# Optimization experiments

Hardware: AMD Instinct MI355X
Metric: run time of the kernel (lower is better)

Reference implementation:

```python
import jax, jax.numpy as jnp
from jax import lax
import numpy as np

B, C, H, W = 16, 128, 128, 128


def setup_inputs() -> dict:
    key = jax.random.key(0)
    k1, k2, k3 = jax.random.split(key, 3)
    x = jax.random.normal(k1, (B, C, H, W), dtype=jnp.float32)
    # depthwise Conv2d(C, C, k=3, padding=1, groups=C): weight (C, 1, 3, 3), bias (C,)
    dw_weight = jax.random.normal(k2, (C, 1, 3, 3), dtype=jnp.float32) * 0.05
    dw_bias = jax.random.normal(k3, (C,), dtype=jnp.float32) * 0.05
    gamma = jnp.zeros((1,), dtype=jnp.float32)  # nn.Parameter(torch.zeros(1))
    return {"x": x, "dw_weight": dw_weight, "dw_bias": dw_bias, "gamma": gamma}


def reference(x, dw_weight, dw_bias, gamma):
    b, c, h, w = x.shape
    f = x.reshape(b, c, h * w)                      # [B, C, N]
    # channel-attention Gram matrix: [B, C, C]
    atten = jnp.einsum('bcn,bdn->bcd', f, f)
    # max-subtract (not softmax): rowwise max minus scores
    atten = jnp.max(atten, axis=-1, keepdims=True) - atten
    # project back to spatial: [B, C, N] -> [B, C, H, W]
    atten = jnp.einsum('bcd,bdn->bcn', atten, f).reshape(b, c, h, w)
    # depthwise 3x3 conv, padding=1
    atten = lax.conv_general_dilated(
        atten, dw_weight,
        window_strides=(1, 1), padding='SAME',
        dimension_numbers=('NCHW', 'OIHW', 'NCHW'),
        feature_group_count=c,
    ) + dw_bias[None, :, None, None]
    # softmax over last dim (W), as torch Softmax(dim=-1) on 4D tensor
    atten = jax.nn.softmax(atten, axis=-1)
    out = gamma * atten + x
    return (out, atten)
```

## Files before the change

kernel.cpp:

```cpp
#include <hip/hip_runtime.h>

#define Bn 16
#define Cn 128
#define Hn 128
#define Wn 128
#define Nn (Hn * Wn)
#define KSPLIT 32

typedef __attribute__((ext_vector_type(8))) short bf16x8;
typedef __attribute__((ext_vector_type(4))) float f32x4;

__device__ __forceinline__ unsigned short bfh(float f) {
    unsigned u = __float_as_uint(f);
    u += 0x7FFFu + ((u >> 16) & 1u);
    return (unsigned short)(u >> 16);
}
__device__ __forceinline__ float bf2f(unsigned short h) {
    return __uint_as_float(((unsigned)h) << 16);
}

__device__ __forceinline__ bf16x8 ldfrag(const unsigned short* S, int row, int quad) {
    return *(const bf16x8*)(S + row * 40 + quad * 8);
}

__global__ __launch_bounds__(256) void colsum_kernel(const float* __restrict__ x,
                                                     float* __restrict__ colsum) {
    const int b = blockIdx.x >> 4;
    const int nt = blockIdx.x & 15;
    const int n4 = (nt << 10) + (threadIdx.x << 2);
    const float* __restrict__ fb = x + (size_t)b * Cn * Nn;
    float4 s = {0.f, 0.f, 0.f, 0.f};
    for (int c = 0; c < Cn; ++c) {
        const float4 v = *(const float4*)(fb + (size_t)c * Nn + n4);
        s.x += v.x; s.y += v.y; s.z += v.z; s.w += v.w;
    }
    *(float4*)(colsum + (size_t)b * Nn + n4) = s;
}

__global__ __launch_bounds__(256, 2) void gram_mfma(const float* __restrict__ x,
                                                    float* __restrict__ Gp) {
    const int bid = blockIdx.x;
    const int ks = bid & 31;
    const int b = bid >> 5;
    const float* __restrict__ fb = x + (size_t)b * Cn * Nn;
    const int k0 = ks << 9;

    __shared__ __align__(16) unsigned short Shi[128 * 40];
    __shared__ __align__(16) unsigned short Slo[128 * 40];

    const int tid = threadIdx.x;
    const int wave = tid >> 6, lane = tid & 63;
    const int m = lane & 15, quad = lane >> 4;
    const int wr = (wave >> 1) << 6;
    const int wc = (wave & 1) << 6;

    f32x4 acc[4][4];
#pragma unroll
    for (int i = 0; i < 4; ++i)
#pragma unroll
        for (int j = 0; j < 4; ++j) acc[i][j] = (f32x4){0.f, 0.f, 0.f, 0.f};

    for (int ck = 0; ck < 512; ck += 32) {
        __syncthreads();
#pragma unroll
        for (int p = 0; p < 4; ++p) {
            const int q = tid + (p << 8);
            const int c = q >> 3;
            const int k4 = (q & 7) << 2;
            const float4 v = *(const float4*)(fb + (size_t)c * Nn + k0 + ck + k4);
            const float f0[4] = {v.x, v.y, v.z, v.w};
            unsigned short h[4], l[4];
#pragma unroll
            for (int e = 0; e < 4; ++e) {
                h[e] = bfh(f0[e]);
                l[e] = bfh(f0[e] - bf2f(h[e]));
            }
            *(ushort4*)(Shi + c * 40 + k4) = make_ushort4(h[0], h[1], h[2], h[3]);
            *(ushort4*)(Slo + c * 40 + k4) = make_ushort4(l[0], l[1], l[2], l[3]);
        }
        __syncthreads();

        bf16x8 Ah[4], Al[4], Bh[4], Bl[4];
#pragma unroll
        for (int i = 0; i < 4; ++i) {
            Ah[i] = ldfrag(Shi, wr + (i << 4) + m, quad);
            Al[i] = ldfrag(Slo, wr + (i << 4) + m, quad);
            Bh[i] = ldfrag(Shi, wc + (i << 4) + m, quad);
            Bl[i] = ldfrag(Slo, wc + (i << 4) + m, quad);
        }
#pragma unroll
        for (int i = 0; i < 4; ++i)
#pragma unroll
            for (int j = 0; j < 4; ++j) {
                acc[i][j] = __builtin_amdgcn_mfma_f32_16x16x32_bf16(Ah[i], Bh[j], acc[i][j], 0, 0, 0);
                acc[i][j] = __builtin_amdgcn_mfma_f32_16x16x32_bf16(Ah[i], Bl[j], acc[i][j], 0, 0, 0);
                acc[i][j] = __builtin_amdgcn_mfma_f32_16x16x32_bf16(Al[i], Bh[j], acc[i][j], 0, 0, 0);
            }
    }

    float* __restrict__ Gb = Gp + (((size_t)ks * Bn + b) << 14);
#pragma unroll
    for (int i = 0; i < 4; ++i)
#pragma unroll
        for (int j = 0; j < 4; ++j)
#pragma unroll
            for (int r = 0; r < 4; ++r) {
                const int row = wr + (i << 4) + (quad << 2) + r;
                const int col = wc + (j << 4) + m;
                Gb[(row << 7) + col] = acc[i][j][r];
            }
}

__global__ __launch_bounds__(128) void prep_kernel(const float* __restrict__ Gp,
                                                   unsigned short* __restrict__ Lhi,
                                                   unsigned short* __restrict__ Llo,
                                                   float* __restrict__ rowmax,
                                                   float* __restrict__ gdiag) {
    const int row = blockIdx.x;
    const int b = row >> 7;
    const int c = row & 127;
    const int t = threadIdx.x;

    const float* __restrict__ p = Gp + (((size_t)b) << 14) + (c << 7) + t;
    float v = 0.0f;
#pragma unroll
    for (int ks = 0; ks < KSPLIT; ++ks)
        v += p[(size_t)ks * ((size_t)Bn << 14)];

    __shared__ float red[128];
    red[t] = v;
    __syncthreads();
#pragma unroll
    for (int s = 64; s > 0; s >>= 1) {
        if (t < s) red[t] = fmaxf(red[t], red[t + s]);
        __syncthreads();
    }
    if (t == 0) rowmax[row] = red[0];
    if (t == c) gdiag[row] = v;
    const float l = (t == c) ? 0.0f : -v;
    const unsigned short h = bfh(l);
    Lhi[(size_t)row * Cn + t] = h;
    Llo[(size_t)row * Cn + t] = bfh(l - bf2f(h));
}

__global__ __launch_bounds__(256, 2) void ymm_mfma(const unsigned short* __restrict__ Lhi,
                                                   const unsigned short* __restrict__ Llo,
                                                   const float* __restrict__ x,
                                                   const float* __restrict__ colsum,
                                                   const float* __restrict__ rowmax,
                                                   const float* __restrict__ gdiag,
                                                   float* __restrict__ Y) {
    const int bid = blockIdx.x;
    const int xcd = bid & 7;
    const int j2 = bid >> 3;
    const int b = (xcd << 1) + (j2 & 1);
    const int nt = j2 >> 1;
    const int n0 = nt << 7;

    const float* __restrict__ fb = x + (size_t)b * Cn * Nn;
    const unsigned short* __restrict__ Lhb = Lhi + (size_t)b * Cn * Cn;
    const unsigned short* __restrict__ Llb = Llo + (size_t)b * Cn * Cn;

    __shared__ __align__(16) unsigned short SAh[128 * 40];
    __shared__ __align__(16) unsigned short SAl[128 * 40];
    __shared__ __align__(16) unsigned short SBh[128 * 40];
    __shared__ __align__(16) unsigned short SBl[128 * 40];

    const int tid = threadIdx.x;
    const int wave = tid >> 6, lane = tid & 63;
    const int m = lane & 15, quad = lane >> 4;
    const int wrc = (wave >> 1) << 6;
    const int wn = (wave & 1) << 6;

    f32x4 acc[4][4];
#pragma unroll
    for (int i = 0; i < 4; ++i)
#pragma unroll
        for (int j = 0; j < 4; ++j) acc[i][j] = (f32x4){0.f, 0.f, 0.f, 0.f};

    for (int dd = 0; dd < Cn; dd += 32) {
        __syncthreads();
#pragma unroll
        for (int p = 0; p < 4; ++p) {
            const int q = tid + (p << 8);
            const int c = q >> 3;
            const int d4 = (q & 7) << 2;
            *(ushort4*)(SAh + c * 40 + d4) = *(const ushort4*)(Lhb + (size_t)c * Cn + dd + d4);
            *(ushort4*)(SAl + c * 40 + d4) = *(const ushort4*)(Llb + (size_t)c * Cn + dd + d4);
        }
#pragma unroll
        for (int p = 0; p < 4; ++p) {
            const int q = tid + (p << 8);
            const int nl = q & 127;
            const int d4 = (q >> 7) << 2;
            unsigned short h[4], l[4];
#pragma unroll
            for (int e = 0; e < 4; ++e) {
                const float f0 = fb[(size_t)(dd + d4 + e) * Nn + n0 + nl];
                h[e] = bfh(f0);
                l[e] = bfh(f0 - bf2f(h[e]));
            }
            *(ushort4*)(SBh + nl * 40 + d4) = make_ushort4(h[0], h[1], h[2], h[3]);
            *(ushort4*)(SBl + nl * 40 + d4) = make_ushort4(l[0], l[1], l[2], l[3]);
        }
        __syncthreads();

        bf16x8 Ah[4], Al[4], Bh[4], Bl[4];
#pragma unroll
        for (int i = 0; i < 4; ++i) {
            Ah[i] = ldfrag(SAh, wrc + (i << 4) + m, quad);
            Al[i] = ldfrag(SAl, wrc + (i << 4) + m, quad);
            Bh[i] = ldfrag(SBh, wn + (i << 4) + m, quad);
            Bl[i] = ldfrag(SBl, wn + (i << 4) + m, quad);
        }
#pragma unroll
        for (int i = 0; i < 4; ++i)
#pragma unroll
            for (int j = 0; j < 4; ++j) {
                acc[i][j] = __builtin_amdgcn_mfma_f32_16x16x32_bf16(Ah[i], Bh[j], acc[i][j], 0, 0, 0);
                acc[i][j] = __builtin_amdgcn_mfma_f32_16x16x32_bf16(Ah[i], Bl[j], acc[i][j], 0, 0, 0);
                acc[i][j] = __builtin_amdgcn_mfma_f32_16x16x32_bf16(Al[i], Bh[j], acc[i][j], 0, 0, 0);
            }
    }

    float* __restrict__ Yb = Y + (size_t)b * Cn * Nn;
#pragma unroll
    for (int i = 0; i < 4; ++i)
#pragma unroll
        for (int r = 0; r < 4; ++r) {
            const int c = wrc + (i << 4) + (quad << 2) + r;
            const float rm = rowmax[(b << 7) + c];
            const float gd = gdiag[(b << 7) + c];
#pragma unroll
            for (int j = 0; j < 4; ++j) {
                const int n = n0 + wn + (j << 4) + m;
                const float cs = colsum[(size_t)b * Nn + n];
                const float fv = fb[(size_t)c * Nn + n];
                Yb[(size_t)c * Nn + n] = fmaf(rm, cs, fmaf(-gd, fv, acc[i][j][r]));
            }
        }
}

__global__ __launch_bounds__(256) void conv_softmax_kernel(const float* __restrict__ Yin,
                                                           const float* __restrict__ wgt,
                                                           const float* __restrict__ bias,
                                                           const float* __restrict__ x,
                                                           const float* __restrict__ gamma,
                                                           float* __restrict__ out,
                                                           float* __restrict__ atten) {
    const int pid = blockIdx.x;
    const int c = pid & (Cn - 1);
    const size_t pbase = (size_t)pid * Nn;

    __shared__ __align__(16) float P[128][131];

    const int tid = threadIdx.x;

#pragma unroll
    for (int p = 0; p < 16; ++p) {
        const int q = tid + (p << 8);
        const int row = q >> 5;
        const int c4 = (q & 31) << 2;
        const float4 v = *(const float4*)(Yin + pbase + (size_t)row * Wn + c4);
        P[row][1 + c4 + 0] = v.x; P[row][1 + c4 + 1] = v.y;
        P[row][1 + c4 + 2] = v.z; P[row][1 + c4 + 3] = v.w;
    }
    if (tid < 128) { P[tid][0] = 0.0f; P[tid][129] = 0.0f; }

    float wk[9];
#pragma unroll
    for (int i = 0; i < 9; ++i) wk[i] = wgt[c * 9 + i];
    const float bs = bias[c];
    const float g = gamma[0];

    __syncthreads();

    const int h = tid >> 1;
    const int c0 = (tid & 1) << 6;

    float acc0[32], acc1[32];
#pragma unroll
    for (int w = 0; w < 32; ++w) { acc0[w] = bs; acc1[w] = bs; }

#pragma unroll
    for (int chunk = 0; chunk < 2; ++chunk) {
        float* acc = chunk ? acc1 : acc0;
        const int cb = c0 + (chunk << 5);
#pragma unroll
        for (int kh = 0; kh < 3; ++kh) {
            const int hh = h + kh - 1;
            if (hh < 0 || hh >= Hn) continue;
            float r[34];
#pragma unroll
            for (int i = 0; i < 34; ++i) r[i] = P[hh][cb + i];
            const float w0 = wk[kh * 3 + 0], w1 = wk[kh * 3 + 1], w2 = wk[kh * 3 + 2];
#pragma unroll
            for (int w = 0; w < 32; ++w)
                acc[w] = fmaf(w0, r[w], fmaf(w1, r[w + 1], fmaf(w2, r[w + 2], acc[w])));
        }
    }

    float m = -1e30f;
#pragma unroll
    for (int w = 0; w < 32; ++w) m = fmaxf(m, fmaxf(acc0[w], acc1[w]));
    m = fmaxf(m, __shfl_xor(m, 1));
    float s = 0.0f;
#pragma unroll
    for (int w = 0; w < 32; ++w) { acc0[w] = __expf(acc0[w] - m); s += acc0[w]; }
#pragma unroll
    for (int w = 0; w < 32; ++w) { acc1[w] = __expf(acc1[w] - m); s += acc1[w]; }
    s += __shfl_xor(s, 1);
    const float inv = 1.0f / s;

    __syncthreads();

#pragma unroll
    for (int w = 0; w < 32; ++w) {
        P[h][1 + c0 + w] = acc0[w] * inv;
        P[h][1 + c0 + 32 + w] = acc1[w] * inv;
    }
    __syncthreads();

#pragma unroll
    for (int p = 0; p < 16; ++p) {
        const int q = tid + (p << 8);
        const int row = q >> 5;
        const int c4 = (q & 31) << 2;
        float4 a;
        a.x = P[row][1 + c4 + 0]; a.y = P[row][1 + c4 + 1];
        a.z = P[row][1 + c4 + 2]; a.w = P[row][1 + c4 + 3];
        const float4 xv = *(const float4*)(x + pbase + (size_t)row * Wn + c4);
        float4 o;
        o.x = fmaf(g, a.x, xv.x); o.y = fmaf(g, a.y, xv.y);
        o.z = fmaf(g, a.z, xv.z); o.w = fmaf(g, a.w, xv.w);
        *(float4*)(atten + pbase + (size_t)row * Wn + c4) = a;
        *(float4*)(out + pbase + (size_t)row * Wn + c4) = o;
    }
}

extern "C" void kernel_launch(void* const* d_in, const int* in_sizes, int n_in,
                              void* d_out, int out_size, void* d_ws, size_t ws_size,
                              hipStream_t stream) {
    const float* x     = (const float*)d_in[0];
    const float* wgt   = (const float*)d_in[1];
    const float* bias  = (const float*)d_in[2];
    const float* gamma = (const float*)d_in[3];

    float* out   = (float*)d_out;
    float* atten = out + (size_t)Bn * Cn * Nn;

    float* Gp = (float*)d_ws;
    float* colsum = Gp + ((size_t)KSPLIT * Bn << 14);
    unsigned short* Lhi = (unsigned short*)(colsum + (size_t)Bn * Nn);
    unsigned short* Llo = Lhi + (size_t)Bn * Cn * Cn;
    float* rowmax = atten;
    float* gdiag  = atten + 2048;

    float* Y = out;

    colsum_kernel<<<Bn * 16, 256, 0, stream>>>(x, colsum);
    gram_mfma<<<Bn * 32, 256, 0, stream>>>(x, Gp);
    prep_kernel<<<Bn * Cn, 128, 0, stream>>>(Gp, Lhi, Llo, rowmax, gdiag);
    ymm_mfma<<<Bn * 128, 256, 0, stream>>>(Lhi, Llo, x, colsum, rowmax, gdiag, Y);
    conv_softmax_kernel<<<Bn * Cn, 256, 0, stream>>>(Y, wgt, bias, x, gamma, out, atten);
}
```

Measured before the change: 525.5 us.

## Fuse column-sum into Gram kernel and load A fragments directly from global

Drops the separate colsum kernel and computes per-column channel sums inside gram_mfma from the float4 values it already loads, reducing them with cross-lane shuffles and a small shared buffer. This removes one full read pass over x (about 128 MB). In ymm_mfma, the L matrix fragments are now read straight from global memory into registers instead of being staged through shared memory. That cuts LDS traffic and shared-memory footprint, at the cost of more uncoalesced global loads from the small L matrices, which are likely cached.

```diff
diff --git a/kernel.cpp b/kernel.cpp
--- a/kernel.cpp
+++ b/kernel.cpp
@@ -23,22 +23,9 @@
     return *(const bf16x8*)(S + row * 40 + quad * 8);
 }
 
-__global__ __launch_bounds__(256) void colsum_kernel(const float* __restrict__ x,
-                                                     float* __restrict__ colsum) {
-    const int b = blockIdx.x >> 4;
-    const int nt = blockIdx.x & 15;
-    const int n4 = (nt << 10) + (threadIdx.x << 2);
-    const float* __restrict__ fb = x + (size_t)b * Cn * Nn;
-    float4 s = {0.f, 0.f, 0.f, 0.f};
-    for (int c = 0; c < Cn; ++c) {
-        const float4 v = *(const float4*)(fb + (size_t)c * Nn + n4);
-        s.x += v.x; s.y += v.y; s.z += v.z; s.w += v.w;
-    }
-    *(float4*)(colsum + (size_t)b * Nn + n4) = s;
-}
-
 __global__ __launch_bounds__(256, 2) void gram_mfma(const float* __restrict__ x,
-                                                    float* __restrict__ Gp) {
+                                                    float* __restrict__ Gp,
+                                                    float* __restrict__ colsum) {
     const int bid = blockIdx.x;
     const int ks = bid & 31;
     const int b = bid >> 5;
@@ -47,6 +34,7 @@
 
     __shared__ __align__(16) unsigned short Shi[128 * 40];
     __shared__ __align__(16) unsigned short Slo[128 * 40];
+    __shared__ float csumW[4][512];
 
     const int tid = threadIdx.x;
     const int wave = tid >> 6, lane = tid & 63;
@@ -62,12 +50,14 @@
 
     for (int ck = 0; ck < 512; ck += 32) {
         __syncthreads();
+        float4 cs = {0.f, 0.f, 0.f, 0.f};
 #pragma unroll
         for (int p = 0; p < 4; ++p) {
             const int q = tid + (p << 8);
             const int c = q >> 3;
             const int k4 = (q & 7) << 2;
             const float4 v = *(const float4*)(fb + (size_t)c * Nn + k0 + ck + k4);
+            cs.x += v.x; cs.y += v.y; cs.z += v.z; cs.w += v.w;
             const float f0[4] = {v.x, v.y, v.z, v.w};
             unsigned short h[4], l[4];
 #pragma unroll
@@ -77,6 +67,17 @@
             }
             *(ushort4*)(Shi + c * 40 + k4) = make_ushort4(h[0], h[1], h[2], h[3]);
             *(ushort4*)(Slo + c * 40 + k4) = make_ushort4(l[0], l[1], l[2], l[3]);
+        }
+#pragma unroll
+        for (int s = 8; s < 64; s <<= 1) {
+            cs.x += __shfl_xor(cs.x, s);
+            cs.y += __shfl_xor(cs.y, s);
+            cs.z += __shfl_xor(cs.z, s);
+            cs.w += __shfl_xor(cs.w, s);
+        }
+        if (lane < 8) {
+            float* dst = &csumW[wave][ck + (lane << 2)];
+            dst[0] = cs.x; dst[1] = cs.y; dst[2] = cs.z; dst[3] = cs.w;
         }
         __syncthreads();
 
@@ -96,6 +97,11 @@
                 acc[i][j] = __builtin_amdgcn_mfma_f32_16x16x32_bf16(Ah[i], Bl[j], acc[i][j], 0, 0, 0);
                 acc[i][j] = __builtin_amdgcn_mfma_f32_16x16x32_bf16(Al[i], Bh[j], acc[i][j], 0, 0, 0);
             }
+    }
+
+    for (int i = tid; i < 512; i += 256) {
+        colsum[(size_t)b * Nn + k0 + i] =
+            csumW[0][i] + csumW[1][i] + csumW[2][i] + csumW[3][i];
     }
 
     float* __restrict__ Gb = Gp + (((size_t)ks * Bn + b) << 14);
@@ -161,8 +167,6 @@
     const unsigned short* __restrict__ Lhb = Lhi + (size_t)b * Cn * Cn;
     const unsigned short* __restrict__ Llb = Llo + (size_t)b * Cn * Cn;
 
-    __shared__ __align__(16) unsigned short SAh[128 * 40];
-    __shared__ __align__(16) unsigned short SAl[128 * 40];
     __shared__ __align__(16) unsigned short SBh[128 * 40];
     __shared__ __align__(16) unsigned short SBl[128 * 40];
 
@@ -179,15 +183,14 @@
         for (int j = 0; j < 4; ++j) acc[i][j] = (f32x4){0.f, 0.f, 0.f, 0.f};
 
     for (int dd = 0; dd < Cn; dd += 32) {
-        __syncthreads();
-#pragma unroll
-        for (int p = 0; p < 4; ++p) {
-            const int q = tid + (p << 8);
-            const int c = q >> 3;
-            const int d4 = (q & 7) << 2;
-            *(ushort4*)(SAh + c * 40 + d4) = *(const ushort4*)(Lhb + (size_t)c * Cn + dd + d4);
-            *(ushort4*)(SAl + c * 40 + d4) = *(const ushort4*)(Llb + (size_t)c * Cn + dd + d4);
-        }
+        bf16x8 Ah[4], Al[4];
+#pragma unroll
+        for (int i = 0; i < 4; ++i) {
+            const size_t ro = (size_t)(wrc + (i << 4) + m) * Cn + dd + (quad << 3);
+            Ah[i] = *(const bf16x8*)(Lhb + ro);
+            Al[i] = *(const bf16x8*)(Llb + ro);
+        }
+        __syncthreads();
 #pragma unroll
         for (int p = 0; p < 4; ++p) {
             const int q = tid + (p << 8);
@@ -205,11 +208,9 @@
         }
         __syncthreads();
 
-        bf16x8 Ah[4], Al[4], Bh[4], Bl[4];
+        bf16x8 Bh[4], Bl[4];
 #pragma unroll
         for (int i = 0; i < 4; ++i) {
-            Ah[i] = ldfrag(SAh, wrc + (i << 4) + m, quad);
-            Al[i] = ldfrag(SAl, wrc + (i << 4) + m, quad);
             Bh[i] = ldfrag(SBh, wn + (i << 4) + m, quad);
             Bl[i] = ldfrag(SBl, wn + (i << 4) + m, quad);
         }
@@ -358,8 +359,7 @@
 
     float* Y = out;
 
-    colsum_kernel<<<Bn * 16, 256, 0, stream>>>(x, colsum);
-    gram_mfma<<<Bn * 32, 256, 0, stream>>>(x, Gp);
+    gram_mfma<<<Bn * 32, 256, 0, stream>>>(x, Gp, colsum);
     prep_kernel<<<Bn * Cn, 128, 0, stream>>>(Gp, Lhi, Llo, rowmax, gdiag);
     ymm_mfma<<<Bn * 128, 256, 0, stream>>>(Lhi, Llo, x, colsum, rowmax, gdiag, Y);
     conv_softmax_kernel<<<Bn * Cn, 256, 0, stream>>>(Y, wgt, bias, x, gamma, out, atten);
```

New measurement: 500.8 us. -4.7%, faster.
